# Optimization experiments

Measured on AMD Instinct MI355X. Metric: run time of the kernel, lower is better.

## Reference

```python
import jax, jax.numpy as jnp
import numpy as np

MARGIN = 5.0
VAR_FLOOR = 1e-4
BIG = 1e6


def setup_inputs() -> dict:
    key = jax.random.key(0)
    ks = jax.random.split(key, 8)
    B, D, R = 512, 768, 128
    C_new, C_old = 10, 100
    return {
        "features": jax.random.normal(ks[0], (B, D), jnp.float32),
        "labels": jax.random.randint(ks[1], (B,), 0, C_new),
        "new_class_ids": jnp.arange(C_new),
        "cur_means": jax.random.normal(ks[2], (C_new, D), jnp.float32),
        "cur_bases": jax.random.normal(ks[3], (C_new, D, R), jnp.float32),
        "cur_variances": jax.random.uniform(ks[4], (C_new, R + 1), jnp.float32),
        "calibrated_old_means": jax.random.normal(ks[5], (C_old, D), jnp.float32),
        "calibrated_old_bases": jax.random.normal(ks[6], (C_old, D, R), jnp.float32),
        "calibrated_old_variances": jax.random.uniform(ks[7], (C_old, R + 1), jnp.float32),
    }


def _geometry_distance_matrix(z, means, bases, variances):
    # z: [B,D], means: [C,D], bases: [C,D,R], variances: [C,R+1] -> [B,C]
    diff = z[:, None, :] - means[None, :, :]                    # [B,C,D]
    coeff = jnp.einsum('bcd,cdr->bcr', diff, bases)             # [B,C,R]
    eig = jnp.maximum(variances[:, :-1], VAR_FLOOR)             # [C,R]
    res = jnp.maximum(variances[:, -1], VAR_FLOOR)              # [C]
    parallel = jnp.sum(coeff * coeff / eig[None, :, :], axis=-1)  # [B,C]
    recon = jnp.einsum('bcr,cdr->bcd', coeff, bases)            # [B,C,D]
    residual_term = jnp.sum((diff - recon) ** 2, axis=-1) / res[None, :]
    dist = (parallel + residual_term) / z.shape[1]              # normalize_by_dim
    return jnp.nan_to_num(dist, nan=BIG, posinf=BIG, neginf=BIG)


def reference(features, labels, new_class_ids, cur_means, cur_bases, cur_variances,
              calibrated_old_means, calibrated_old_bases, calibrated_old_variances):
    z = jnp.nan_to_num(features, nan=0.0, posinf=0.0, neginf=0.0)  # [B,D]
    labels = labels.reshape(-1)

    own_all = _geometry_distance_matrix(z, cur_means, cur_bases, cur_variances)  # [B,C_new_total]
    old_all = _geometry_distance_matrix(z, calibrated_old_means, calibrated_old_bases,
                                        calibrated_old_variances)               # [B,C_old]
    old_min = jnp.min(old_all, axis=1)                                           # [B]

    # Per-new-class masks; union of class masks reproduces new_mask implicitly.
    masks = (labels[None, :] == new_class_ids[:, None]).astype(z.dtype)          # [K,B]
    counts = masks.sum(axis=1)                                                   # [K]
    denom = jnp.maximum(counts, 1.0)

    own_k = own_all[:, new_class_ids].T                                          # [K,B]
    hinge = jax.nn.relu(MARGIN + own_k - old_min[None, :])                       # [K,B]

    total_k = (hinge * masks).sum(axis=1) / denom
    own_k_mean = (own_k * masks).sum(axis=1) / denom
    old_k_mean = (old_min[None, :] * masks).sum(axis=1) / denom

    valid = (counts > 0).astype(z.dtype)
    n_valid = jnp.maximum(valid.sum(), 1.0)
    total = (total_k * valid).sum() / n_valid
    own = (own_k_mean * valid).sum() / n_valid
    old = (old_k_mean * valid).sum() / n_valid
    return jnp.stack([total, own, old])  # [total, own, old]
```

## Files before the change

kernel.cpp:

```cpp
#include <hip/hip_runtime.h>
#include <hip/hip_bf16.h>
#include <math.h>
#include <stdint.h>

#define B_N   512
#define D_N   768
#define R_N   128
#define C_NEW 10
#define C_OLD 100
#define C_TOT 110
#define MARGIN_F    5.0f
#define VAR_FLOOR_F 1e-4f
#define BIG_F       1e6f

typedef __bf16 bf16;
typedef __bf16 bf16x4 __attribute__((ext_vector_type(4)));
typedef __bf16 bf16x8 __attribute__((ext_vector_type(8)));
typedef float  f32x4  __attribute__((ext_vector_type(4)));

__device__ __forceinline__ float cleanf(float v) { return isfinite(v) ? v : 0.0f; }

__device__ __forceinline__ unsigned encf(float f) {
    unsigned u = __float_as_uint(f);
    return (u & 0x80000000u) ? ~u : (u | 0x80000000u);
}
__device__ __forceinline__ float decf(unsigned u) {
    return (u & 0x80000000u) ? __uint_as_float(u & 0x7fffffffu) : __uint_as_float(~u);
}

#define GL16(gp, lp)                                                            \
    __builtin_amdgcn_global_load_lds(                                           \
        (const __attribute__((address_space(1))) unsigned int*)(gp),            \
        (__attribute__((address_space(3))) unsigned int*)(lp), 16, 0, 0)

__device__ __forceinline__ int swz_elem(int D, int row) {
    int k0 = D & ~63;
    int g  = (D >> 3) & 7;
    return k0 + (((g ^ (row & 7))) << 3) + (D & 7);
}

__global__ __launch_bounds__(256, 2)
void prep_all(const float* __restrict__ z,
              const float* __restrict__ cur_means, const float* __restrict__ old_means,
              const float* __restrict__ cur_bases, const float* __restrict__ old_bases,
              bf16* __restrict__ zbf, float* __restrict__ znorm,
              float* __restrict__ munorm, float* __restrict__ m_c,
              bf16* __restrict__ basesT, bf16* __restrict__ G,
              unsigned* __restrict__ ominE)
{
    const int bid = blockIdx.x, t = threadIdx.x;
    __shared__ __align__(16) unsigned char lds[33280];
    const int wave = t >> 6, lane = t & 63;

    if (bid < 128) {
        if (bid == 0) {
            ominE[t] = 0xFFFFFFFFu;
            ominE[256 + t] = 0xFFFFFFFFu;
        }
        const int b = bid * 4 + wave;
        const float4* src = (const float4*)(z + (size_t)b * D_N);
        bf16* dst = zbf + (size_t)b * D_N;
        float nrm = 0.f;
        #pragma unroll
        for (int i = 0; i < 3; ++i) {
            const int D = (lane + i * 64) * 4;
            float4 v = src[lane + i * 64];
            v.x = cleanf(v.x); v.y = cleanf(v.y); v.z = cleanf(v.z); v.w = cleanf(v.w);
            nrm += v.x * v.x + v.y * v.y + v.z * v.z + v.w * v.w;
            bf16x4 w;
            w[0] = (bf16)v.x; w[1] = (bf16)v.y; w[2] = (bf16)v.z; w[3] = (bf16)v.w;
            *(bf16x4*)(dst + swz_elem(D, b)) = w;
        }
        #pragma unroll
        for (int off = 32; off >= 1; off >>= 1) nrm += __shfl_xor(nrm, off, 64);
        if (lane == 0) znorm[b] = nrm;
        return;
    }

    if (bid < 128 + C_TOT) {
        const int c = bid - 128;
        const float* Bc = (c < C_NEW) ? cur_bases + (size_t)c * D_N * R_N
                                      : old_bases + (size_t)(c - C_NEW) * D_N * R_N;
        const float* mu = (c < C_NEW) ? cur_means + (size_t)c * D_N
                                      : old_means + (size_t)(c - C_NEW) * D_N;
        bf16*  sT   = (bf16*)lds;
        float* sMuF = (float*)(lds + 18432);
        float* sRed = (float*)(lds + 18432 + 256);
        const int quad = lane >> 4, l15 = lane & 15;
        const int wrg = (wave >> 1) * 64, wsg = (wave & 1) * 64;
        const int rg = t & 31, dgq = t >> 5;

        f32x4 acc[4][4];
        #pragma unroll
        for (int i = 0; i < 4; ++i)
            #pragma unroll
            for (int j = 0; j < 4; ++j) acc[i][j] = (f32x4)0.0f;
        float mAcc = 0.f, muN = 0.f;

        float4 pf[8];
        #pragma unroll
        for (int i = 0; i < 2; ++i) {
            const int dg = i * 8 + dgq;
            const float* src = Bc + (size_t)(dg * 4) * R_N + rg * 4;
            #pragma unroll
            for (int m = 0; m < 4; ++m) pf[i * 4 + m] = *(const float4*)(src + m * R_N);
        }

        for (int kc = 0; kc < 12; ++kc) {
            const int k0 = kc * 64;
            __syncthreads();
            #pragma unroll
            for (int i = 0; i < 2; ++i) {
                const int dg = i * 8 + dgq;
                #pragma unroll
                for (int j = 0; j < 4; ++j) {
                    const int R = rg * 4 + j;
                    bf16x4 w;
                    w[0] = (bf16)pf[i * 4 + 0][j];
                    w[1] = (bf16)pf[i * 4 + 1][j];
                    w[2] = (bf16)pf[i * 4 + 2][j];
                    w[3] = (bf16)pf[i * 4 + 3][j];
                    *(bf16x4*)(sT + R * 72 + dg * 4) = w;
                }
            }
            if (t < 64) {
                float mv = mu[k0 + t];
                sMuF[t] = mv;
                muN += mv * mv;
            }
            if (kc < 11) {
                #pragma unroll
                for (int i = 0; i < 2; ++i) {
                    const int dg = i * 8 + dgq;
                    const float* src = Bc + (size_t)((kc + 1) * 64 + dg * 4) * R_N + rg * 4;
                    #pragma unroll
                    for (int m = 0; m < 4; ++m) pf[i * 4 + m] = *(const float4*)(src + m * R_N);
                }
            }
            __syncthreads();
            #pragma unroll
            for (int kk = 0; kk < 64; kk += 32) {
                bf16x8 af[4], bg[4];
                #pragma unroll
                for (int i = 0; i < 4; ++i) af[i] = *(const bf16x8*)(sT + (wrg + 16 * i + l15) * 72 + kk + quad * 8);
                #pragma unroll
                for (int j = 0; j < 4; ++j) bg[j] = *(const bf16x8*)(sT + (wsg + 16 * j + l15) * 72 + kk + quad * 8);
                #pragma unroll
                for (int i = 0; i < 4; ++i)
                    #pragma unroll
                    for (int j = 0; j < 4; ++j)
                        acc[i][j] = __builtin_amdgcn_mfma_f32_16x16x32_bf16(af[i], bg[j], acc[i][j], 0, 0, 0);
            }
            {
                const int rr = t >> 1, hf = t & 1;
                const bf16* tr = sT + rr * 72 + hf * 32;
                const float* mf = sMuF + hf * 32;
                #pragma unroll
                for (int m = 0; m < 4; ++m) {
                    bf16x8 v = *(const bf16x8*)(tr + m * 8);
                    #pragma unroll
                    for (int e = 0; e < 8; ++e) mAcc += (float)v[e] * mf[m * 8 + e];
                }
            }
        }
        #pragma unroll
        for (int i = 0; i < 4; ++i)
            #pragma unroll
            for (int j = 0; j < 4; ++j)
                #pragma unroll
                for (int reg = 0; reg < 4; ++reg) {
                    int r = wrg + 16 * i + quad * 4 + reg;
                    int s = wsg + 16 * j + l15;
                    G[(size_t)c * 16384 + (size_t)r * 128 + s] = (bf16)acc[i][j][reg];
                }
        sRed[t] = mAcc;
        __syncthreads();
        if (t < 128) m_c[c * R_N + t] = sRed[2 * t] + sRed[2 * t + 1];
        if (t < 64) {
            #pragma unroll
            for (int off = 32; off >= 1; off >>= 1) muN += __shfl_xor(muN, off, 64);
            if (lane == 0) munorm[c] = muN;
        }
        return;
    }

    const int tb = bid - (128 + C_TOT);
    const int dt = tb % 6, c = tb / 6;
    const float* Bc = (c < C_NEW) ? cur_bases + (size_t)c * D_N * R_N
                                  : old_bases + (size_t)(c - C_NEW) * D_N * R_N;
    bf16 (*T)[128] = (bf16(*)[128])lds;
    const int d0 = dt * 128;
    const int rg  = t & 31;
    const int dgb = t >> 5;

    #pragma unroll
    for (int i = 0; i < 4; ++i) {
        const int dg = i * 8 + dgb;
        const float* src = Bc + (size_t)(d0 + dg * 4) * R_N + rg * 4;
        float4 v0 = *(const float4*)(src);
        float4 v1 = *(const float4*)(src + R_N);
        float4 v2 = *(const float4*)(src + 2 * R_N);
        float4 v3 = *(const float4*)(src + 3 * R_N);
        const float* f0 = (const float*)&v0;
        const float* f1 = (const float*)&v1;
        const float* f2 = (const float*)&v2;
        const float* f3 = (const float*)&v3;
        #pragma unroll
        for (int j = 0; j < 4; ++j) {
            const int R = rg * 4 + j;
            const int pc = dg ^ (R & 31);
            bf16x4 w;
            w[0] = (bf16)f0[j]; w[1] = (bf16)f1[j]; w[2] = (bf16)f2[j]; w[3] = (bf16)f3[j];
            *(bf16x4*)(&T[R][pc * 4]) = w;
        }
    }
    __syncthreads();

    #pragma unroll
    for (int it = 0; it < 16; ++it) {
        const int q = it * 256 + t;
        const int r = q >> 5, u = q & 31;
        const int pc = u ^ (r & 31);
        ushort4 w = *(const ushort4*)(&T[r][pc * 4]);
        const int D = d0 + u * 4;
        *(ushort4*)(basesT + (size_t)c * R_N * D_N + (size_t)r * D_N + swz_elem(D, r)) = w;
    }
}

#define PADC 136
#define SM_A    0
#define SM_B    8192
#define SM_C    0
#define SM_MU   24576
#define SM_M    26112
#define SM_INV  26624
#define SM_Q    27136
#define SM_PAR  27392
#define SM_CN   27648
#define SM_ZD   27904
#define SM_T2   28160
#define SM_SZ   30208

__global__ __launch_bounds__(256, 4)
void main_dist(const bf16* __restrict__ zbf, const bf16* __restrict__ basesT,
               const bf16* __restrict__ G, const float* __restrict__ m_c,
               const float* __restrict__ cur_vars, const float* __restrict__ old_vars,
               const float* __restrict__ cur_means, const float* __restrict__ old_means,
               const float* __restrict__ znorm, const float* __restrict__ munorm,
               float* __restrict__ gdist, unsigned* __restrict__ ominE)
{
    const int fid = blockIdx.x;
    const int x = fid & 7;
    const int y = (fid % 112) >> 3;
    const int mt = fid / 112;
    const int c = x + 8 * y;
    if (c >= C_TOT) return;

    __shared__ __align__(16) unsigned char smem[SM_SZ];
    unsigned char* sAb = smem + SM_A;
    unsigned char* sBb = smem + SM_B;
    bf16*  sC   = (bf16*)(smem + SM_C);
    bf16*  sMuB = (bf16*)(smem + SM_MU);
    float* sM   = (float*)(smem + SM_M);
    float* sInv = (float*)(smem + SM_INV);
    float* sQ   = (float*)(smem + SM_Q);
    float* sPar = (float*)(smem + SM_PAR);
    float* sCn  = (float*)(smem + SM_CN);
    float* sZd  = (float*)(smem + SM_ZD);
    float* sT2  = (float*)(smem + SM_T2);

    const int tid = threadIdx.x, wave = tid >> 6, lane = tid & 63;
    const int quad = lane >> 4, l15 = lane & 15;
    const int wr  = (wave >> 1) * 32;
    const int wcc = (wave & 1) * 64;

    const int b0 = mt * 64;
    const float* vars = (c < C_NEW) ? cur_vars + (size_t)c * (R_N + 1)
                                    : old_vars + (size_t)(c - C_NEW) * (R_N + 1);
    const float* mu = (c < C_NEW) ? cur_means + (size_t)c * D_N
                                  : old_means + (size_t)(c - C_NEW) * D_N;

    if (tid < 128) {
        sM[tid]   = m_c[c * R_N + tid];
        sInv[tid] = 1.0f / fmaxf(vars[tid], VAR_FLOOR_F);
    }
    if (tid < 64) sQ[tid] = 0.0f;
    for (int i = tid; i < D_N; i += 256) sMuB[i] = (bf16)mu[i];

    f32x4 acc1[2][4];
    #pragma unroll
    for (int i = 0; i < 2; ++i)
        #pragma unroll
        for (int j = 0; j < 4; ++j) acc1[i][j] = (f32x4)0.0f;
    float zd = 0.f;
    const int zrow = tid >> 2, zpart = tid & 3;

    const char* BbB = (const char*)basesT + (size_t)c * (R_N * D_N * 2);
    const char* AzB = (const char*)zbf + (size_t)b0 * (D_N * 2);
    const int offRC = (wave * 8 + (lane >> 3)) * (D_N * 2) + (lane & 7) * 16;
    char* ldsB = (char*)sBb + wave * 1024;
    char* ldsA = (char*)sAb + wave * 1024;

    for (int kc = 0; kc < 12; ++kc) {
        const int kb = kc * 128;
        const int k0 = kc * 64;
        __syncthreads();
        #pragma unroll
        for (int p = 0; p < 4; ++p)
            GL16(BbB + offRC + p * (32 * D_N * 2) + kb, ldsB + p * 4096);
        #pragma unroll
        for (int q = 0; q < 2; ++q)
            GL16(AzB + offRC + q * (32 * D_N * 2) + kb, ldsA + q * 4096);
        __syncthreads();
        #pragma unroll
        for (int kk = 0; kk < 64; kk += 32) {
            const int gbase = kk >> 3;
            bf16x8 af[2], bg[4];
            #pragma unroll
            for (int i = 0; i < 2; ++i) {
                const int rowA = wr + 16 * i + l15;
                af[i] = *(const bf16x8*)(sAb + rowA * 128 + (((gbase + quad) ^ (rowA & 7)) << 4));
            }
            #pragma unroll
            for (int j = 0; j < 4; ++j) {
                const int rowB = wcc + 16 * j + l15;
                bg[j] = *(const bf16x8*)(sBb + rowB * 128 + (((gbase + quad) ^ (rowB & 7)) << 4));
            }
            #pragma unroll
            for (int i = 0; i < 2; ++i)
                #pragma unroll
                for (int j = 0; j < 4; ++j)
                    acc1[i][j] = __builtin_amdgcn_mfma_f32_16x16x32_bf16(af[i], bg[j], acc1[i][j], 0, 0, 0);
        }
        #pragma unroll
        for (int gg = 0; gg < 2; ++gg) {
            const int g = zpart * 2 + gg;
            bf16x8 a = *(const bf16x8*)(sAb + zrow * 128 + ((g ^ (zrow & 7)) << 4));
            bf16x8 b = *(const bf16x8*)(sMuB + k0 + g * 8);
            #pragma unroll
            for (int e = 0; e < 8; ++e) zd += (float)a[e] * (float)b[e];
        }
    }

    zd += __shfl_xor(zd, 1, 64);
    zd += __shfl_xor(zd, 2, 64);
    if ((tid & 3) == 0) sZd[zrow] = zd;
    __syncthreads();

    #pragma unroll
    for (int j = 0; j < 4; ++j) {
        float mcv = sM[wcc + 16 * j + l15];
        #pragma unroll
        for (int i = 0; i < 2; ++i)
            #pragma unroll
            for (int reg = 0; reg < 4; ++reg)
                sC[(wr + 16 * i + quad * 4 + reg) * PADC + wcc + 16 * j + l15] =
                    (bf16)(acc1[i][j][reg] - mcv);
    }
    __syncthreads();

    {
        int row = tid >> 2, qtr = tid & 3;
        float par = 0.f, cn = 0.f;
        #pragma unroll
        for (int m = 0; m < 4; ++m) {
            bf16x8 v = *(const bf16x8*)(sC + row * PADC + qtr * 32 + m * 8);
            #pragma unroll
            for (int e = 0; e < 8; ++e) {
                float f = (float)v[e];
                int col = qtr * 32 + m * 8 + e;
                cn  += f * f;
                par += f * f * sInv[col];
            }
        }
        sT2[tid] = par;
        sT2[256 + tid] = cn;
    }
    __syncthreads();
    if (tid < 64) {
        sPar[tid] = sT2[tid * 4] + sT2[tid * 4 + 1] + sT2[tid * 4 + 2] + sT2[tid * 4 + 3];
        sCn[tid]  = sT2[256 + tid * 4] + sT2[256 + tid * 4 + 1]
                  + sT2[256 + tid * 4 + 2] + sT2[256 + tid * 4 + 3];
    }

    const bf16* Gc = G + (size_t)c * 16384;
    f32x4 acc2[2][4];
    #pragma unroll
    for (int i = 0; i < 2; ++i)
        #pragma unroll
        for (int j = 0; j < 4; ++j) acc2[i][j] = (f32x4)0.0f;
    #pragma unroll
    for (int kc4 = 0; kc4 < 4; ++kc4) {
        const int kb = kc4 * 32;
        bf16x8 af[2], bg[4];
        #pragma unroll
        for (int i = 0; i < 2; ++i) af[i] = *(const bf16x8*)(sC + (wr + 16 * i + l15) * PADC + kb + quad * 8);
        #pragma unroll
        for (int j = 0; j < 4; ++j) bg[j] = *(const bf16x8*)(Gc + (size_t)(wcc + 16 * j + l15) * 128 + kb + quad * 8);
        #pragma unroll
        for (int i = 0; i < 2; ++i)
            #pragma unroll
            for (int j = 0; j < 4; ++j)
                acc2[i][j] = __builtin_amdgcn_mfma_f32_16x16x32_bf16(af[i], bg[j], acc2[i][j], 0, 0, 0);
    }

    #pragma unroll
    for (int i = 0; i < 2; ++i)
        #pragma unroll
        for (int reg = 0; reg < 4; ++reg) {
            const int row = wr + 16 * i + quad * 4 + reg;
            float qp = 0.f;
            #pragma unroll
            for (int j = 0; j < 4; ++j)
                qp += acc2[i][j][reg] * (float)sC[row * PADC + wcc + 16 * j + l15];
            qp += __shfl_xor(qp, 1, 64);
            qp += __shfl_xor(qp, 2, 64);
            qp += __shfl_xor(qp, 4, 64);
            qp += __shfl_xor(qp, 8, 64);
            if (l15 == 0) atomicAdd(&sQ[row], qp);
        }
    __syncthreads();

    if (tid < 64) {
        int b = b0 + tid;
        float nd2 = znorm[b] - 2.0f * sZd[tid] + munorm[c];
        float res = fmaxf(vars[R_N], VAR_FLOOR_F);
        float dist = (sPar[tid] + (nd2 - 2.0f * sCn[tid] + sQ[tid]) / res) / (float)D_N;
        if (!isfinite(dist)) dist = BIG_F;
        if (c < C_NEW) {
            gdist[(size_t)b * C_NEW + c] = dist;
        } else {
            atomicMin(ominE + b, encf(dist));
        }
    }
}

__global__ __launch_bounds__(512)
void finalize(const float* __restrict__ gdist, const unsigned* __restrict__ ominE,
              const int* __restrict__ labels, const int* __restrict__ ncid,
              float* __restrict__ out)
{
    __shared__ float acc[C_NEW * 4];
    __shared__ int sNcid[C_NEW];
    const int t = threadIdx.x;
    if (t < C_NEW * 4) acc[t] = 0.f;
    if (t < C_NEW) sNcid[t] = ncid[t];
    __syncthreads();

    {
        float mn = decf(ominE[t]);
        const int lab = labels[t];
        #pragma unroll
        for (int k = 0; k < C_NEW; ++k) {
            if (lab == sNcid[k]) {
                int col = min(max(sNcid[k], 0), C_NEW - 1);
                float ow = gdist[(size_t)t * C_NEW + col];
                atomicAdd(&acc[k * 4 + 0], 1.0f);
                atomicAdd(&acc[k * 4 + 1], fmaxf(0.0f, MARGIN_F + ow - mn));
                atomicAdd(&acc[k * 4 + 2], ow);
                atomicAdd(&acc[k * 4 + 3], mn);
            }
        }
    }
    __syncthreads();

    if (t == 0) {
        float total = 0.f, own = 0.f, old = 0.f, nv = 0.f;
        #pragma unroll
        for (int k = 0; k < C_NEW; ++k) {
            float cnt = acc[k * 4 + 0];
            float den = fmaxf(cnt, 1.0f);
            if (cnt > 0.f) {
                nv += 1.f;
                total += acc[k * 4 + 1] / den;
                own   += acc[k * 4 + 2] / den;
                old   += acc[k * 4 + 3] / den;
            }
        }
        float nvd = fmaxf(nv, 1.0f);
        out[0] = total / nvd;
        out[1] = own / nvd;
        out[2] = old / nvd;
    }
}

extern "C" void kernel_launch(void* const* d_in, const int* in_sizes, int n_in,
                              void* d_out, int out_size, void* d_ws, size_t ws_size,
                              hipStream_t stream)
{
    const float* features  = (const float*)d_in[0];
    const int*   labels    = (const int*)d_in[1];
    const int*   ncid      = (const int*)d_in[2];
    const float* cur_means = (const float*)d_in[3];
    const float* cur_bases = (const float*)d_in[4];
    const float* cur_vars  = (const float*)d_in[5];
    const float* old_means = (const float*)d_in[6];
    const float* old_bases = (const float*)d_in[7];
    const float* old_vars  = (const float*)d_in[8];

    unsigned char* ws = (unsigned char*)d_ws;
    float*    gdist  = (float*)(ws + 0);
    unsigned* ominE  = (unsigned*)(ws + 20480);
    bf16*     zbf    = (bf16*) (ws + 22528);
    float*    znorm  = (float*)(ws + 808960);
    float*    munorm = (float*)(ws + 811008);
    float*    m_c    = (float*)(ws + 811520);
    bf16*     basesT = (bf16*) (ws + 867840);
    bf16*     G      = (bf16*) (ws + 22494720);

    prep_all<<<dim3(128 + C_TOT + 6 * C_TOT), dim3(256), 0, stream>>>(
        features, cur_means, old_means, cur_bases, old_bases,
        zbf, znorm, munorm, m_c, basesT, G, ominE);
    main_dist<<<dim3(896), dim3(256), 0, stream>>>(zbf, basesT, G, m_c,
                                                   cur_vars, old_vars,
                                                   cur_means, old_means,
                                                   znorm, munorm,
                                                   gdist, ominE);
    finalize<<<dim3(1), dim3(512), 0, stream>>>(gdist, ominE, labels, ncid,
                                                (float*)d_out);
}
```

Measured before the change: 156.6 us.

## Fuse bases transpose into Gram-matrix prep blocks to avoid rereading bases

The separate transpose blocks, which reread each class's fp32 basis and wrote a swizzled bf16 transposed copy, are removed. The Gram-computing blocks now write the transposed rows from their LDS tile while they accumulate the mean projection, so each basis is read from HBM once instead of twice. The grid shrinks from 898 to 238 blocks, which cuts parallelism: each of the 110 class blocks now does more serial work, and it also issues the basesT stores.

```diff
diff --git a/kernel.cpp b/kernel.cpp
--- a/kernel.cpp
+++ b/kernel.cpp
@@ -40,16 +40,16 @@
 }
 
 __global__ __launch_bounds__(256, 2)
-void prep_all(const float* __restrict__ z,
-              const float* __restrict__ cur_means, const float* __restrict__ old_means,
-              const float* __restrict__ cur_bases, const float* __restrict__ old_bases,
-              bf16* __restrict__ zbf, float* __restrict__ znorm,
-              float* __restrict__ munorm, float* __restrict__ m_c,
-              bf16* __restrict__ basesT, bf16* __restrict__ G,
-              unsigned* __restrict__ ominE)
+void prep_fused(const float* __restrict__ z,
+                const float* __restrict__ cur_means, const float* __restrict__ old_means,
+                const float* __restrict__ cur_bases, const float* __restrict__ old_bases,
+                bf16* __restrict__ zbf, float* __restrict__ znorm,
+                float* __restrict__ munorm, float* __restrict__ m_c,
+                bf16* __restrict__ basesT, bf16* __restrict__ G,
+                unsigned* __restrict__ ominE)
 {
     const int bid = blockIdx.x, t = threadIdx.x;
-    __shared__ __align__(16) unsigned char lds[33280];
+    __shared__ __align__(16) unsigned char lds[18432 + 256 + 1024];
     const int wave = t >> 6, lane = t & 63;
 
     if (bid < 128) {
@@ -77,153 +77,110 @@
         return;
     }
 
-    if (bid < 128 + C_TOT) {
-        const int c = bid - 128;
-        const float* Bc = (c < C_NEW) ? cur_bases + (size_t)c * D_N * R_N
-                                      : old_bases + (size_t)(c - C_NEW) * D_N * R_N;
-        const float* mu = (c < C_NEW) ? cur_means + (size_t)c * D_N
-                                      : old_means + (size_t)(c - C_NEW) * D_N;
-        bf16*  sT   = (bf16*)lds;
-        float* sMuF = (float*)(lds + 18432);
-        float* sRed = (float*)(lds + 18432 + 256);
-        const int quad = lane >> 4, l15 = lane & 15;
-        const int wrg = (wave >> 1) * 64, wsg = (wave & 1) * 64;
-        const int rg = t & 31, dgq = t >> 5;
-
-        f32x4 acc[4][4];
-        #pragma unroll
-        for (int i = 0; i < 4; ++i)
-            #pragma unroll
-            for (int j = 0; j < 4; ++j) acc[i][j] = (f32x4)0.0f;
-        float mAcc = 0.f, muN = 0.f;
-
-        float4 pf[8];
+    const int c = bid - 128;
+    const float* Bc = (c < C_NEW) ? cur_bases + (size_t)c * D_N * R_N
+                                  : old_bases + (size_t)(c - C_NEW) * D_N * R_N;
+    const float* mu = (c < C_NEW) ? cur_means + (size_t)c * D_N
+                                  : old_means + (size_t)(c - C_NEW) * D_N;
+    bf16*  sT   = (bf16*)lds;
+    float* sMuF = (float*)(lds + 18432);
+    float* sRed = (float*)(lds + 18432 + 256);
+    const int quad = lane >> 4, l15 = lane & 15;
+    const int wrg = (wave >> 1) * 64, wsg = (wave & 1) * 64;
+    const int rg = t & 31, dgq = t >> 5;
+
+    f32x4 acc[4][4];
+    #pragma unroll
+    for (int i = 0; i < 4; ++i)
+        #pragma unroll
+        for (int j = 0; j < 4; ++j) acc[i][j] = (f32x4)0.0f;
+    float mAcc = 0.f, muN = 0.f;
+
+    float4 pf[8];
+    #pragma unroll
+    for (int i = 0; i < 2; ++i) {
+        const int dg = i * 8 + dgq;
+        const float* src = Bc + (size_t)(dg * 4) * R_N + rg * 4;
+        #pragma unroll
+        for (int m = 0; m < 4; ++m) pf[i * 4 + m] = *(const float4*)(src + m * R_N);
+    }
+
+    for (int kc = 0; kc < 12; ++kc) {
+        const int k0 = kc * 64;
+        __syncthreads();
         #pragma unroll
         for (int i = 0; i < 2; ++i) {
             const int dg = i * 8 + dgq;
-            const float* src = Bc + (size_t)(dg * 4) * R_N + rg * 4;
-            #pragma unroll
-            for (int m = 0; m < 4; ++m) pf[i * 4 + m] = *(const float4*)(src + m * R_N);
-        }
-
-        for (int kc = 0; kc < 12; ++kc) {
-            const int k0 = kc * 64;
-            __syncthreads();
+            #pragma unroll
+            for (int j = 0; j < 4; ++j) {
+                const int R = rg * 4 + j;
+                bf16x4 w;
+                w[0] = (bf16)pf[i * 4 + 0][j];
+                w[1] = (bf16)pf[i * 4 + 1][j];
+                w[2] = (bf16)pf[i * 4 + 2][j];
+                w[3] = (bf16)pf[i * 4 + 3][j];
+                *(bf16x4*)(sT + R * 72 + dg * 4) = w;
+            }
+        }
+        if (t < 64) {
+            float mv = mu[k0 + t];
+            sMuF[t] = mv;
+            muN += mv * mv;
+        }
+        if (kc < 11) {
             #pragma unroll
             for (int i = 0; i < 2; ++i) {
                 const int dg = i * 8 + dgq;
+                const float* src = Bc + (size_t)((kc + 1) * 64 + dg * 4) * R_N + rg * 4;
                 #pragma unroll
-                for (int j = 0; j < 4; ++j) {
-                    const int R = rg * 4 + j;
-                    bf16x4 w;
-                    w[0] = (bf16)pf[i * 4 + 0][j];
-                    w[1] = (bf16)pf[i * 4 + 1][j];
-                    w[2] = (bf16)pf[i * 4 + 2][j];
-                    w[3] = (bf16)pf[i * 4 + 3][j];
-                    *(bf16x4*)(sT + R * 72 + dg * 4) = w;
-                }
-            }
-            if (t < 64) {
-                float mv = mu[k0 + t];
-                sMuF[t] = mv;
-                muN += mv * mv;
-            }
-            if (kc < 11) {
+                for (int m = 0; m < 4; ++m) pf[i * 4 + m] = *(const float4*)(src + m * R_N);
+            }
+        }
+        __syncthreads();
+        #pragma unroll
+        for (int kk = 0; kk < 64; kk += 32) {
+            bf16x8 af[4], bg[4];
+            #pragma unroll
+            for (int i = 0; i < 4; ++i) af[i] = *(const bf16x8*)(sT + (wrg + 16 * i + l15) * 72 + kk + quad * 8);
+            #pragma unroll
+            for (int j = 0; j < 4; ++j) bg[j] = *(const bf16x8*)(sT + (wsg + 16 * j + l15) * 72 + kk + quad * 8);
+            #pragma unroll
+            for (int i = 0; i < 4; ++i)
                 #pragma unroll
-                for (int i = 0; i < 2; ++i) {
-                    const int dg = i * 8 + dgq;
-                    const float* src = Bc + (size_t)((kc + 1) * 64 + dg * 4) * R_N + rg * 4;
-                    #pragma unroll
-                    for (int m = 0; m < 4; ++m) pf[i * 4 + m] = *(const float4*)(src + m * R_N);
-                }
-            }
-            __syncthreads();
-            #pragma unroll
-            for (int kk = 0; kk < 64; kk += 32) {
-                bf16x8 af[4], bg[4];
+                for (int j = 0; j < 4; ++j)
+                    acc[i][j] = __builtin_amdgcn_mfma_f32_16x16x32_bf16(af[i], bg[j], acc[i][j], 0, 0, 0);
+        }
+        {
+            const int rr = t >> 1, hf = t & 1;
+            const float* mf = sMuF + hf * 32;
+            bf16* dstRow = basesT + (size_t)c * R_N * D_N + (size_t)rr * D_N + k0;
+            #pragma unroll
+            for (int m = 0; m < 4; ++m) {
+                const int g = hf * 4 + m;
+                bf16x8 v = *(const bf16x8*)(sT + rr * 72 + g * 8);
                 #pragma unroll
-                for (int i = 0; i < 4; ++i) af[i] = *(const bf16x8*)(sT + (wrg + 16 * i + l15) * 72 + kk + quad * 8);
-                #pragma unroll
-                for (int j = 0; j < 4; ++j) bg[j] = *(const bf16x8*)(sT + (wsg + 16 * j + l15) * 72 + kk + quad * 8);
-                #pragma unroll
-                for (int i = 0; i < 4; ++i)
-                    #pragma unroll
-                    for (int j = 0; j < 4; ++j)
-                        acc[i][j] = __builtin_amdgcn_mfma_f32_16x16x32_bf16(af[i], bg[j], acc[i][j], 0, 0, 0);
-            }
-            {
-                const int rr = t >> 1, hf = t & 1;
-                const bf16* tr = sT + rr * 72 + hf * 32;
-                const float* mf = sMuF + hf * 32;
-                #pragma unroll
-                for (int m = 0; m < 4; ++m) {
-                    bf16x8 v = *(const bf16x8*)(tr + m * 8);
-                    #pragma unroll
-                    for (int e = 0; e < 8; ++e) mAcc += (float)v[e] * mf[m * 8 + e];
-                }
-            }
-        }
-        #pragma unroll
-        for (int i = 0; i < 4; ++i)
-            #pragma unroll
-            for (int j = 0; j < 4; ++j)
-                #pragma unroll
-                for (int reg = 0; reg < 4; ++reg) {
-                    int r = wrg + 16 * i + quad * 4 + reg;
-                    int s = wsg + 16 * j + l15;
-                    G[(size_t)c * 16384 + (size_t)r * 128 + s] = (bf16)acc[i][j][reg];
-                }
-        sRed[t] = mAcc;
-        __syncthreads();
-        if (t < 128) m_c[c * R_N + t] = sRed[2 * t] + sRed[2 * t + 1];
-        if (t < 64) {
-            #pragma unroll
-            for (int off = 32; off >= 1; off >>= 1) muN += __shfl_xor(muN, off, 64);
-            if (lane == 0) munorm[c] = muN;
-        }
-        return;
-    }
-
-    const int tb = bid - (128 + C_TOT);
-    const int dt = tb % 6, c = tb / 6;
-    const float* Bc = (c < C_NEW) ? cur_bases + (size_t)c * D_N * R_N
-                                  : old_bases + (size_t)(c - C_NEW) * D_N * R_N;
-    bf16 (*T)[128] = (bf16(*)[128])lds;
-    const int d0 = dt * 128;
-    const int rg  = t & 31;
-    const int dgb = t >> 5;
-
-    #pragma unroll
-    for (int i = 0; i < 4; ++i) {
-        const int dg = i * 8 + dgb;
-        const float* src = Bc + (size_t)(d0 + dg * 4) * R_N + rg * 4;
-        float4 v0 = *(const float4*)(src);
-        float4 v1 = *(const float4*)(src + R_N);
-        float4 v2 = *(const float4*)(src + 2 * R_N);
-        float4 v3 = *(const float4*)(src + 3 * R_N);
-        const float* f0 = (const float*)&v0;
-        const float* f1 = (const float*)&v1;
-        const float* f2 = (const float*)&v2;
-        const float* f3 = (const float*)&v3;
-        #pragma unroll
-        for (int j = 0; j < 4; ++j) {
-            const int R = rg * 4 + j;
-            const int pc = dg ^ (R & 31);
-            bf16x4 w;
-            w[0] = (bf16)f0[j]; w[1] = (bf16)f1[j]; w[2] = (bf16)f2[j]; w[3] = (bf16)f3[j];
-            *(bf16x4*)(&T[R][pc * 4]) = w;
-        }
-    }
-    __syncthreads();
-
-    #pragma unroll
-    for (int it = 0; it < 16; ++it) {
-        const int q = it * 256 + t;
-        const int r = q >> 5, u = q & 31;
-        const int pc = u ^ (r & 31);
-        ushort4 w = *(const ushort4*)(&T[r][pc * 4]);
-        const int D = d0 + u * 4;
-        *(ushort4*)(basesT + (size_t)c * R_N * D_N + (size_t)r * D_N + swz_elem(D, r)) = w;
+                for (int e = 0; e < 8; ++e) mAcc += (float)v[e] * mf[m * 8 + e];
+                *(bf16x8*)(dstRow + ((g ^ (rr & 7)) << 3)) = v;
+            }
+        }
+    }
+    #pragma unroll
+    for (int i = 0; i < 4; ++i)
+        #pragma unroll
+        for (int j = 0; j < 4; ++j)
+            #pragma unroll
+            for (int reg = 0; reg < 4; ++reg) {
+                int r = wrg + 16 * i + quad * 4 + reg;
+                int s = wsg + 16 * j + l15;
+                G[(size_t)c * 16384 + (size_t)r * 128 + s] = (bf16)acc[i][j][reg];
+            }
+    sRed[t] = mAcc;
+    __syncthreads();
+    if (t < 128) m_c[c * R_N + t] = sRed[2 * t] + sRed[2 * t + 1];
+    if (t < 64) {
+        #pragma unroll
+        for (int off = 32; off >= 1; off >>= 1) muN += __shfl_xor(muN, off, 64);
+        if (lane == 0) munorm[c] = muN;
     }
 }
 
@@ -508,7 +465,7 @@
     bf16*     basesT = (bf16*) (ws + 867840);
     bf16*     G      = (bf16*) (ws + 22494720);
 
-    prep_all<<<dim3(128 + C_TOT + 6 * C_TOT), dim3(256), 0, stream>>>(
+    prep_fused<<<dim3(128 + C_TOT), dim3(256), 0, stream>>>(
         features, cur_means, old_means, cur_bases, old_bases,
         zbf, znorm, munorm, m_c, basesT, G, ominE);
     main_dist<<<dim3(896), dim3(256), 0, stream>>>(zbf, basesT, G, m_c,
```

After: 161.9 us. +3.3%, slower.
